# Performance work log

Hardware: AMD Instinct MI355X
Metric: run time of the kernel (lower is better)

## Reference

```python
import jax, jax.numpy as jnp
import numpy as np
from jax import lax

B, C, H, W = 8, 4, 256, 256
INF = 1e6  # 'no zero in this column' sentinel distance


def _column_dist(f):
    # f: [N, H, W] binary (1 = foreground). Returns per-pixel distance along
    # axis H to the nearest zero in the same column (INF if none).
    ft = jnp.moveaxis(f, 1, 0)  # [H, N, W]

    def step(carry, row):
        d = jnp.where(row == 0, 0.0, jnp.minimum(carry + 1.0, INF))
        return d, d

    init = jnp.full(ft.shape[1:], INF, dtype=jnp.float32)
    _, df = lax.scan(step, init, ft)            # scan down
    _, db = lax.scan(step, init, ft[::-1])      # scan up
    g = jnp.minimum(df, db[::-1])               # [H, N, W]
    return jnp.moveaxis(g, 0, 1)                # [N, H, W]


def _edt(y):
    # Exact 2D Euclidean distance transform of binary images y: [N, H, W].
    # Matches scipy.ndimage.distance_transform_edt: distance of each nonzero
    # pixel to the nearest zero pixel. Separable: 1D column distance, then an
    # exact min-plus over rows: D2[i, x] = min_j (g[i, j]^2 + (x - j)^2).
    g2 = _column_dist(y) ** 2                   # [N, H, W]
    j = jnp.arange(W, dtype=jnp.float32)
    offs = (j[:, None] - j[None, :]) ** 2       # [x, j]

    def per_image(g2i):                         # g2i: [H, W]
        d2 = jnp.min(g2i[:, None, :] + offs[None, :, :], axis=-1)  # [H, W]
        return jnp.sqrt(d2)

    # lax.map keeps peak memory at one [H, W, W] envelope per image.
    return lax.map(per_image, g2)               # [N, H, W]


def _rrwmap(y_):
    # One-hot scatter: y[b, c, h, w] = 1 iff y_[b, 0, h, w] == c
    onehot = (y_[:, 0, :, :, None] == jnp.arange(C)).astype(jnp.float32)
    onehot = jnp.moveaxis(onehot, -1, 1)        # [B, C, H, W]
    d = _edt(onehot.reshape(B * C, H, W)).reshape(B, C, H, W)
    mx = jnp.max(d, axis=(2, 3), keepdims=True)
    r = -d / (mx + 1e-15)
    # rrwmap[rrwmap == 0] = 1  (background pixels, where d == 0 -> -0.0)
    return jnp.where(r == 0, 1.0, r)


def setup_inputs() -> dict:
    key = jax.random.key(0)
    k1, k2 = jax.random.split(key)
    x = jax.random.normal(k1, (B, C, H, W), dtype=jnp.float32)
    y_ = jax.random.randint(k2, (B, 1, H, W), 0, C, dtype=jnp.int32)
    return {"x": x, "y_": y_}


def reference(x, y_):
    p = jax.nn.softmax(x, axis=1)
    return jnp.mean(p * _rrwmap(y_))
```

## Files before the change

kernel.cpp:

```cpp
#include <hip/hip_runtime.h>

#define B_ 8
#define C_ 4
#define H_ 256
#define W_ 256
#define NIMG 32
#define HW 65536
#define NROW 2048
#define INF2 (1.0e6f * 1.0e6f)

__global__ __launch_bounds__(256) void fused_kernel(const int* __restrict__ y,
                                                    const float* __restrict__ x,
                                                    float* __restrict__ P) {
    const int row = blockIdx.x;
    const int b = row >> 8;
    const int h = row & (H_ - 1);
    const int tx = threadIdx.x;
    const int* __restrict__ yb = y + b * HW;

    const float* __restrict__ xb = x + (size_t)b * (C_ * HW) + h * W_ + tx;
    const float x0 = xb[0];
    const float x1 = xb[HW];
    const float x2 = xb[2 * HW];
    const float x3 = xb[3 * HW];
    const int yv = yb[h * W_ + tx];
    int nbu[4], nbd[4];
#pragma unroll
    for (int k = 1; k <= 4; ++k) {
        nbu[k - 1] = yb[max(h - k, 0) * W_ + tx];
        nbd[k - 1] = yb[min(h + k, H_ - 1) * W_ + tx];
    }

    float g2 = INF2;
    bool done = false;
#pragma unroll
    for (int k = 1; k <= 4; ++k) {
        const bool hit = ((h - k >= 0) && nbu[k - 1] != yv) ||
                         ((h + k < H_) && nbd[k - 1] != yv);
        if (!done && hit) { g2 = (float)(k * k); done = true; }
    }
    if (__any(!done)) {
        for (int k = 5; k < H_; ++k) {
            const int hu = h - k, hd = h + k;
            const int u = yb[max(hu, 0) * W_ + tx];
            const int dn = yb[min(hd, H_ - 1) * W_ + tx];
            const bool hit = ((hu >= 0) && u != yv) || ((hd < H_) && dn != yv);
            if (!done && hit) { g2 = (float)(k * k); done = true; }
            if (__all(done)) break;
            if (hu < 0 && hd >= H_) break;
        }
    }

    __shared__ uint2 s2[W_];
    s2[tx] = make_uint2(__float_as_uint(g2), (unsigned)yv);
    __syncthreads();

    const unsigned cu = (unsigned)yv;
    float m = g2;
#define CAND(J, K2) ({ int j_ = (J); j_ = min(max(j_, 0), W_ - 1);            \
                       const uint2 v_ = s2[j_];                               \
                       (((v_.y == cu) ? __uint_as_float(v_.x) : 0.0f) + (K2)); })
    m = fminf(m, fminf(CAND(tx - 1, 1.0f),  CAND(tx + 1, 1.0f)));
    m = fminf(m, fminf(CAND(tx - 2, 4.0f),  CAND(tx + 2, 4.0f)));
    m = fminf(m, fminf(CAND(tx - 3, 9.0f),  CAND(tx + 3, 9.0f)));
    m = fminf(m, fminf(CAND(tx - 4, 16.0f), CAND(tx + 4, 16.0f)));
    if (__any(m > 25.0f)) {
        float k2 = 25.0f, tk1 = 11.0f;
        for (int k = 5; k < W_; ++k) {
            m = fminf(m, fminf(CAND(tx - k, k2), CAND(tx + k, k2)));
            k2 += tk1; tk1 += 2.0f;
            if (__all(k2 >= m)) break;
        }
    }
#undef CAND
    const float d = sqrtf(m);

    const float xm = fmaxf(fmaxf(x0, x1), fmaxf(x2, x3));
    const float e0 = __expf(x0 - xm), e1 = __expf(x1 - xm);
    const float e2 = __expf(x2 - xm), e3 = __expf(x3 - xm);
    const float se = e0 + e1 + e2 + e3;
    const float inv = 1.0f / se;
    const float ec = (yv == 0) ? e0 : (yv == 1) ? e1 : (yv == 2) ? e2 : e3;
    const float p = ec * inv;
    float T = (se - ec) * inv;
    const float a = p * d;

    float A0 = (yv == 0) ? a : 0.0f, M0 = (yv == 0) ? d : 0.0f;
    float A1 = (yv == 1) ? a : 0.0f, M1 = (yv == 1) ? d : 0.0f;
    float A2 = (yv == 2) ? a : 0.0f, M2 = (yv == 2) ? d : 0.0f;
    float A3 = (yv == 3) ? a : 0.0f, M3 = (yv == 3) ? d : 0.0f;

#pragma unroll
    for (int off = 1; off < 64; off <<= 1) {
        A0 += __shfl_xor(A0, off); A1 += __shfl_xor(A1, off);
        A2 += __shfl_xor(A2, off); A3 += __shfl_xor(A3, off);
        T  += __shfl_xor(T,  off);
        M0 = fmaxf(M0, __shfl_xor(M0, off)); M1 = fmaxf(M1, __shfl_xor(M1, off));
        M2 = fmaxf(M2, __shfl_xor(M2, off)); M3 = fmaxf(M3, __shfl_xor(M3, off));
    }
    __shared__ float red[4][9];
    const int wid = tx >> 6;
    if ((tx & 63) == 0) {
        red[wid][0] = A0; red[wid][1] = A1; red[wid][2] = A2; red[wid][3] = A3;
        red[wid][4] = M0; red[wid][5] = M1; red[wid][6] = M2; red[wid][7] = M3;
        red[wid][8] = T;
    }
    __syncthreads();
    if (tx < 9) {
        const float v0 = red[0][tx], v1 = red[1][tx], v2 = red[2][tx], v3 = red[3][tx];
        const float r = (tx >= 4 && tx < 8) ? fmaxf(fmaxf(v0, v1), fmaxf(v2, v3))
                                            : (v0 + v1) + (v2 + v3);
        P[tx * NROW + row] = r;
    }
}

__global__ void finish_kernel(const float* __restrict__ P, float* __restrict__ out) {
    const int t = threadIdx.x;
    const int g = t >> 3, l = t & 7;
    const int b = g >> 2, c = g & 3;
    const float* Pa = P + c * NROW + b * H_;
    const float* Pm = P + (4 + c) * NROW + b * H_;
    float a = 0.0f, mm = 0.0f;
#pragma unroll 8
    for (int i = 0; i < 32; ++i) {
        a += Pa[l + (i << 3)];
        mm = fmaxf(mm, Pm[l + (i << 3)]);
    }
#pragma unroll
    for (int off = 1; off < 8; off <<= 1) {
        a += __shfl_xor(a, off);
        mm = fmaxf(mm, __shfl_xor(mm, off));
    }
    float tt = 0.0f;
    const float* Pt = P + 8 * NROW;
#pragma unroll
    for (int i = 0; i < 8; ++i) tt += Pt[t + (i << 8)];
#pragma unroll
    for (int off = 1; off < 64; off <<= 1) tt += __shfl_xor(tt, off);
    __shared__ float sV[32];
    __shared__ float sT[4];
    if (l == 0) sV[g] = a / (mm + 1e-15f);
    if ((t & 63) == 0) sT[t >> 6] = tt;
    __syncthreads();
    if (t == 0) {
        float S = 0.0f;
#pragma unroll
        for (int i = 0; i < 32; ++i) S += sV[i];
        const float T = (sT[0] + sT[1]) + (sT[2] + sT[3]);
        out[0] = (T - S) * (1.0f / 2097152.0f);
    }
}

extern "C" void kernel_launch(void* const* d_in, const int* in_sizes, int n_in,
                              void* d_out, int out_size, void* d_ws, size_t ws_size,
                              hipStream_t stream) {
    const float* x = (const float*)d_in[0];
    const int* y = (const int*)d_in[1];
    float* out = (float*)d_out;
    float* P = (float*)d_ws;

    fused_kernel<<<NROW, 256, 0, stream>>>(y, x, P);
    finish_kernel<<<1, 256, 0, stream>>>(P, out);
}
```

Measured before the change: 17.18 us.

## Process four rows per block and share the vertical neighbour window

Each block now handles four consecutive image rows instead of one, loading a shared 12-row window of labels into registers so that neighbouring rows reuse the vertical-scan loads. The cross-row reductions are accumulated in registers before the wave shuffle, and the partial-sum buffer shrinks four-fold, so the finish kernel reads less. The aim is fewer redundant global loads and fewer blocks and reductions. The cost is less parallelism (512 blocks instead of 2048) and per-row __any/__all fallback loops that now run serially inside one block.

```diff
diff --git a/kernel.cpp b/kernel.cpp
--- a/kernel.cpp
+++ b/kernel.cpp
@@ -6,103 +6,135 @@
 #define W_ 256
 #define NIMG 32
 #define HW 65536
-#define NROW 2048
+#define RPB 4
+#define NBLK (B_ * H_ / RPB)
 #define INF2 (1.0e6f * 1.0e6f)
 
 __global__ __launch_bounds__(256) void fused_kernel(const int* __restrict__ y,
                                                     const float* __restrict__ x,
                                                     float* __restrict__ P) {
-    const int row = blockIdx.x;
-    const int b = row >> 8;
-    const int h = row & (H_ - 1);
+    const int blk = blockIdx.x;
+    const int b = blk >> 6;
+    const int h0 = (blk & 63) * RPB;
     const int tx = threadIdx.x;
     const int* __restrict__ yb = y + b * HW;
 
-    const float* __restrict__ xb = x + (size_t)b * (C_ * HW) + h * W_ + tx;
-    const float x0 = xb[0];
-    const float x1 = xb[HW];
-    const float x2 = xb[2 * HW];
-    const float x3 = xb[3 * HW];
-    const int yv = yb[h * W_ + tx];
-    int nbu[4], nbd[4];
+    int yr[12];
 #pragma unroll
-    for (int k = 1; k <= 4; ++k) {
-        nbu[k - 1] = yb[max(h - k, 0) * W_ + tx];
-        nbd[k - 1] = yb[min(h + k, H_ - 1) * W_ + tx];
+    for (int i = 0; i < 12; ++i) {
+        const int hh = min(max(h0 - 4 + i, 0), H_ - 1);
+        yr[i] = yb[hh * W_ + tx];
+    }
+    float xv[RPB][C_];
+    const float* __restrict__ xb = x + (size_t)b * (C_ * HW) + h0 * W_ + tx;
+#pragma unroll
+    for (int r = 0; r < RPB; ++r)
+#pragma unroll
+        for (int c = 0; c < C_; ++c) xv[r][c] = xb[c * HW + r * W_];
+
+    float g2v[RPB];
+#pragma unroll
+    for (int r = 0; r < RPB; ++r) {
+        const int yv = yr[4 + r];
+        const int h = h0 + r;
+        float g2 = INF2;
+        bool done = false;
+#pragma unroll
+        for (int k = 1; k <= 4; ++k) {
+            const bool hit = ((h - k >= 0) && yr[4 + r - k] != yv) ||
+                             ((h + k < H_) && yr[4 + r + k] != yv);
+            if (!done && hit) { g2 = (float)(k * k); done = true; }
+        }
+        if (__any(!done)) {
+            for (int k = 5; k < H_; ++k) {
+                const int hu = h - k, hd = h + k;
+                const int u = yb[max(hu, 0) * W_ + tx];
+                const int dn = yb[min(hd, H_ - 1) * W_ + tx];
+                const bool hit = ((hu >= 0) && u != yv) || ((hd < H_) && dn != yv);
+                if (!done && hit) { g2 = (float)(k * k); done = true; }
+                if (__all(done)) break;
+                if (hu < 0 && hd >= H_) break;
+            }
+        }
+        g2v[r] = g2;
     }
 
-    float g2 = INF2;
-    bool done = false;
+    __shared__ uint2 s2[RPB][W_];
 #pragma unroll
-    for (int k = 1; k <= 4; ++k) {
-        const bool hit = ((h - k >= 0) && nbu[k - 1] != yv) ||
-                         ((h + k < H_) && nbd[k - 1] != yv);
-        if (!done && hit) { g2 = (float)(k * k); done = true; }
+    for (int r = 0; r < RPB; ++r)
+        s2[r][tx] = make_uint2(__float_as_uint(g2v[r]), (unsigned)yr[4 + r]);
+    __syncthreads();
+
+#define CAND(SR, CU, J, K2) ({ int j_ = (J); j_ = min(max(j_, 0), W_ - 1);     \
+                               const uint2 v_ = (SR)[j_];                      \
+                               (((v_.y == (CU)) ? __uint_as_float(v_.x) : 0.0f) + (K2)); })
+    float mv[RPB];
+#pragma unroll
+    for (int r = 0; r < RPB; ++r) {
+        const unsigned cu = (unsigned)yr[4 + r];
+        const uint2* sr = s2[r];
+        float m = g2v[r];
+        m = fminf(m, fminf(CAND(sr, cu, tx - 1, 1.0f),  CAND(sr, cu, tx + 1, 1.0f)));
+        m = fminf(m, fminf(CAND(sr, cu, tx - 2, 4.0f),  CAND(sr, cu, tx + 2, 4.0f)));
+        m = fminf(m, fminf(CAND(sr, cu, tx - 3, 9.0f),  CAND(sr, cu, tx + 3, 9.0f)));
+        m = fminf(m, fminf(CAND(sr, cu, tx - 4, 16.0f), CAND(sr, cu, tx + 4, 16.0f)));
+        mv[r] = m;
     }
-    if (__any(!done)) {
-        for (int k = 5; k < H_; ++k) {
-            const int hu = h - k, hd = h + k;
-            const int u = yb[max(hu, 0) * W_ + tx];
-            const int dn = yb[min(hd, H_ - 1) * W_ + tx];
-            const bool hit = ((hu >= 0) && u != yv) || ((hd < H_) && dn != yv);
-            if (!done && hit) { g2 = (float)(k * k); done = true; }
-            if (__all(done)) break;
-            if (hu < 0 && hd >= H_) break;
+#pragma unroll
+    for (int r = 0; r < RPB; ++r) {
+        if (__any(mv[r] > 25.0f)) {
+            const unsigned cu = (unsigned)yr[4 + r];
+            const uint2* sr = s2[r];
+            float m = mv[r];
+            float k2 = 25.0f, tk1 = 11.0f;
+            for (int k = 5; k < W_; ++k) {
+                m = fminf(m, fminf(CAND(sr, cu, tx - k, k2), CAND(sr, cu, tx + k, k2)));
+                k2 += tk1; tk1 += 2.0f;
+                if (__all(k2 >= m)) break;
+            }
+            mv[r] = m;
+        }
+    }
+#undef CAND
+
+    float A[C_] = {0.f, 0.f, 0.f, 0.f};
+    float M[C_] = {0.f, 0.f, 0.f, 0.f};
+    float T = 0.0f;
+#pragma unroll
+    for (int r = 0; r < RPB; ++r) {
+        const int yv = yr[4 + r];
+        const float d = sqrtf(mv[r]);
+        const float x0 = xv[r][0], x1 = xv[r][1], x2 = xv[r][2], x3 = xv[r][3];
+        const float xm = fmaxf(fmaxf(x0, x1), fmaxf(x2, x3));
+        const float e0 = __expf(x0 - xm), e1 = __expf(x1 - xm);
+        const float e2 = __expf(x2 - xm), e3 = __expf(x3 - xm);
+        const float se = e0 + e1 + e2 + e3;
+        const float inv = 1.0f / se;
+        const float ec = (yv == 0) ? e0 : (yv == 1) ? e1 : (yv == 2) ? e2 : e3;
+        const float p = ec * inv;
+        T += (se - ec) * inv;
+        const float a = p * d;
+#pragma unroll
+        for (int c = 0; c < C_; ++c) {
+            A[c] += (yv == c) ? a : 0.0f;
+            M[c] = fmaxf(M[c], (yv == c) ? d : 0.0f);
         }
     }
 
-    __shared__ uint2 s2[W_];
-    s2[tx] = make_uint2(__float_as_uint(g2), (unsigned)yv);
-    __syncthreads();
-
-    const unsigned cu = (unsigned)yv;
-    float m = g2;
-#define CAND(J, K2) ({ int j_ = (J); j_ = min(max(j_, 0), W_ - 1);            \
-                       const uint2 v_ = s2[j_];                               \
-                       (((v_.y == cu) ? __uint_as_float(v_.x) : 0.0f) + (K2)); })
-    m = fminf(m, fminf(CAND(tx - 1, 1.0f),  CAND(tx + 1, 1.0f)));
-    m = fminf(m, fminf(CAND(tx - 2, 4.0f),  CAND(tx + 2, 4.0f)));
-    m = fminf(m, fminf(CAND(tx - 3, 9.0f),  CAND(tx + 3, 9.0f)));
-    m = fminf(m, fminf(CAND(tx - 4, 16.0f), CAND(tx + 4, 16.0f)));
-    if (__any(m > 25.0f)) {
-        float k2 = 25.0f, tk1 = 11.0f;
-        for (int k = 5; k < W_; ++k) {
-            m = fminf(m, fminf(CAND(tx - k, k2), CAND(tx + k, k2)));
-            k2 += tk1; tk1 += 2.0f;
-            if (__all(k2 >= m)) break;
-        }
-    }
-#undef CAND
-    const float d = sqrtf(m);
-
-    const float xm = fmaxf(fmaxf(x0, x1), fmaxf(x2, x3));
-    const float e0 = __expf(x0 - xm), e1 = __expf(x1 - xm);
-    const float e2 = __expf(x2 - xm), e3 = __expf(x3 - xm);
-    const float se = e0 + e1 + e2 + e3;
-    const float inv = 1.0f / se;
-    const float ec = (yv == 0) ? e0 : (yv == 1) ? e1 : (yv == 2) ? e2 : e3;
-    const float p = ec * inv;
-    float T = (se - ec) * inv;
-    const float a = p * d;
-
-    float A0 = (yv == 0) ? a : 0.0f, M0 = (yv == 0) ? d : 0.0f;
-    float A1 = (yv == 1) ? a : 0.0f, M1 = (yv == 1) ? d : 0.0f;
-    float A2 = (yv == 2) ? a : 0.0f, M2 = (yv == 2) ? d : 0.0f;
-    float A3 = (yv == 3) ? a : 0.0f, M3 = (yv == 3) ? d : 0.0f;
-
 #pragma unroll
     for (int off = 1; off < 64; off <<= 1) {
-        A0 += __shfl_xor(A0, off); A1 += __shfl_xor(A1, off);
-        A2 += __shfl_xor(A2, off); A3 += __shfl_xor(A3, off);
-        T  += __shfl_xor(T,  off);
-        M0 = fmaxf(M0, __shfl_xor(M0, off)); M1 = fmaxf(M1, __shfl_xor(M1, off));
-        M2 = fmaxf(M2, __shfl_xor(M2, off)); M3 = fmaxf(M3, __shfl_xor(M3, off));
+#pragma unroll
+        for (int c = 0; c < C_; ++c) {
+            A[c] += __shfl_xor(A[c], off);
+            M[c] = fmaxf(M[c], __shfl_xor(M[c], off));
+        }
+        T += __shfl_xor(T, off);
     }
     __shared__ float red[4][9];
     const int wid = tx >> 6;
     if ((tx & 63) == 0) {
-        red[wid][0] = A0; red[wid][1] = A1; red[wid][2] = A2; red[wid][3] = A3;
-        red[wid][4] = M0; red[wid][5] = M1; red[wid][6] = M2; red[wid][7] = M3;
+#pragma unroll
+        for (int c = 0; c < C_; ++c) { red[wid][c] = A[c]; red[wid][4 + c] = M[c]; }
         red[wid][8] = T;
     }
     __syncthreads();
@@ -110,7 +142,7 @@
         const float v0 = red[0][tx], v1 = red[1][tx], v2 = red[2][tx], v3 = red[3][tx];
         const float r = (tx >= 4 && tx < 8) ? fmaxf(fmaxf(v0, v1), fmaxf(v2, v3))
                                             : (v0 + v1) + (v2 + v3);
-        P[tx * NROW + row] = r;
+        P[tx * NBLK + blk] = r;
     }
 }
 
@@ -118,11 +150,11 @@
     const int t = threadIdx.x;
     const int g = t >> 3, l = t & 7;
     const int b = g >> 2, c = g & 3;
-    const float* Pa = P + c * NROW + b * H_;
-    const float* Pm = P + (4 + c) * NROW + b * H_;
+    const float* Pa = P + c * NBLK + b * 64;
+    const float* Pm = P + (4 + c) * NBLK + b * 64;
     float a = 0.0f, mm = 0.0f;
-#pragma unroll 8
-    for (int i = 0; i < 32; ++i) {
+#pragma unroll
+    for (int i = 0; i < 8; ++i) {
         a += Pa[l + (i << 3)];
         mm = fmaxf(mm, Pm[l + (i << 3)]);
     }
@@ -131,10 +163,8 @@
         a += __shfl_xor(a, off);
         mm = fmaxf(mm, __shfl_xor(mm, off));
     }
-    float tt = 0.0f;
-    const float* Pt = P + 8 * NROW;
-#pragma unroll
-    for (int i = 0; i < 8; ++i) tt += Pt[t + (i << 8)];
+    const float* Pt = P + 8 * NBLK;
+    float tt = Pt[t] + Pt[t + 256];
 #pragma unroll
     for (int off = 1; off < 64; off <<= 1) tt += __shfl_xor(tt, off);
     __shared__ float sV[32];
@@ -159,6 +189,6 @@
     float* out = (float*)d_out;
     float* P = (float*)d_ws;
 
-    fused_kernel<<<NROW, 256, 0, stream>>>(y, x, P);
+    fused_kernel<<<NBLK, 256, 0, stream>>>(y, x, P);
     finish_kernel<<<1, 256, 0, stream>>>(P, out);
 }
```

After: 15.07 us (median of 2 runs). -12.2%, faster.
